# Performance work log

Hardware: AMD Instinct MI355X
Metric: run time of the kernel (lower is better)

The kernel has to match this reference:

```python
import jax, jax.numpy as jnp
import numpy as np

B, T, D, H = 2, 2048, 2048, 16
HD = D // H  # 128
HALF = HD // 2  # 64


def _apply_rotary(x, cos, sin):
    """x: (B,H,T,HD); cos/sin: (T, HD//2). Interleaved rotation matching torch ref."""
    half = x.shape[-1] // 2
    x1, x2 = x[..., :half], x[..., half:]
    c = cos[None, None, :, :]
    s = sin[None, None, :, :]
    # stack on last axis then flatten -> out[...,2i]=x1*c-x2*s, out[...,2i+1]=x1*s+x2*c
    return jnp.stack([x1 * c - x2 * s, x1 * s + x2 * c], axis=-1).reshape(x.shape)


def setup_inputs() -> dict:
    key = jax.random.key(0)
    k1, k2, k3 = jax.random.split(key, 3)
    x = jax.random.normal(k1, (B, T, D), dtype=jnp.float32)
    # realistic RoPE tables: theta = 10000^{-2i/HD}
    inv_freq = 1.0 / (10000.0 ** (np.arange(0, HALF, dtype=np.float32) * 2.0 / HD))
    ang = np.arange(T, dtype=np.float32)[:, None] * inv_freq[None, :]  # (T, HALF)
    cos = jnp.asarray(np.cos(ang), dtype=jnp.float32)
    sin = jnp.asarray(np.sin(ang), dtype=jnp.float32)
    Wqkv = jax.random.normal(k2, (D, 3 * D), dtype=jnp.float32) * (D ** -0.5)
    Wproj = jax.random.normal(k3, (D, D), dtype=jnp.float32) * (D ** -0.5)
    return {"x": x, "cos": cos, "sin": sin, "Wqkv": Wqkv, "Wproj": Wproj}


def reference(x, cos, sin, Wqkv, Wproj):
    b, t, d = x.shape
    qkv = (x @ Wqkv).reshape(b, t, 3, H, HD)
    q = jnp.transpose(qkv[:, :, 0], (0, 2, 1, 3))  # (B,H,T,HD)
    k = jnp.transpose(qkv[:, :, 1], (0, 2, 1, 3))
    v = jnp.transpose(qkv[:, :, 2], (0, 2, 1, 3))
    q = _apply_rotary(q, cos, sin)
    k = _apply_rotary(k, cos, sin)
    scale = 1.0 / jnp.sqrt(jnp.asarray(HD, dtype=x.dtype))
    scores = jnp.einsum("bhqd,bhkd->bhqk", q, k) * scale
    causal = jnp.tril(jnp.ones((t, t), dtype=bool))
    scores = jnp.where(causal[None, None], scores, jnp.finfo(x.dtype).min)
    attn = jax.nn.softmax(scores, axis=-1)
    out = jnp.einsum("bhqk,bhkd->bhqd", attn, v)
    out = jnp.transpose(out, (0, 2, 1, 3)).reshape(b, t, d)
    return out @ Wproj
```

## Files before the change

### kernel.cpp

```cpp
#include <hip/hip_runtime.h>
#include <hip/hip_bf16.h>

#define B_  2
#define T_  2048
#define D_  2048
#define H_  16
#define HD_ 128
#define NT_ 4096
#define D3_ 6144

typedef __bf16 bf16;
typedef _Float16 f16;
typedef bf16 bf16x2 __attribute__((ext_vector_type(2)));
typedef bf16 bf16x4 __attribute__((ext_vector_type(4)));
typedef bf16 bf16x8 __attribute__((ext_vector_type(8)));
typedef f16  f16x2  __attribute__((ext_vector_type(2)));
typedef f16  f16x4  __attribute__((ext_vector_type(4)));
typedef float floatx4 __attribute__((ext_vector_type(4)));

__device__ __forceinline__ void gl_lds16(const void* g, void* l) {
    __builtin_amdgcn_global_load_lds((const __attribute__((address_space(1))) void*)g,
                                     (__attribute__((address_space(3))) void*)l, 16, 0, 0);
}

__global__ __launch_bounds__(256) void k_prep(const float* __restrict__ x,
                                              const float* __restrict__ Wqkv, const float* __restrict__ Wproj,
                                              bf16* __restrict__ xb, bf16* __restrict__ WqkvT, bf16* __restrict__ WprojT) {
    int blk = blockIdx.x;
    int tid = threadIdx.x;
    if (blk < 8192) {
        int i = blk * 256 + tid;
        float4 v = ((const float4*)x)[i];
        bf16x4 o = { (bf16)v.x, (bf16)v.y, (bf16)v.z, (bf16)v.w };
        ((bf16x4*)xb)[i] = o;
        return;
    }
    __shared__ float tile[64][65];
    const float* in; bf16* out; int C, bx;
    if (blk < 8192 + 3072) { bx = blk - 8192; in = Wqkv; out = WqkvT; C = D3_; }
    else                   { bx = blk - 8192 - 3072; in = Wproj; out = WprojT; C = D_; }
    const int R = D_;
    int nbx = C / 64;
    int c0 = (bx % nbx) * 64, r0 = (bx / nbx) * 64;
#pragma unroll
    for (int i = 0; i < 16; i++) {
        int idx = tid + i * 256, r = idx >> 6, c = idx & 63;
        tile[r][c] = in[(size_t)(r0 + r) * C + (c0 + c)];
    }
    __syncthreads();
#pragma unroll
    for (int i = 0; i < 16; i++) {
        int idx = tid + i * 256, r = idx >> 6, c = idx & 63;
        out[(size_t)(c0 + r) * R + (r0 + c)] = (bf16)tile[c][r];
    }
}

__global__ __launch_bounds__(256) void k_gemm_qkv(const bf16* __restrict__ A, const bf16* __restrict__ Bt,
                                                  const float* __restrict__ cosp, const float* __restrict__ sinp,
                                                  bf16* __restrict__ Qg, bf16* __restrict__ Kg, f16* __restrict__ VTg) {
    __shared__ bf16 As[128 * 32];
    __shared__ bf16 Bs[128 * 32];
    __shared__ bf16 stage[128 * 130];
    const int tid = threadIdx.x, w = tid >> 6, lane = tid & 63;
    const int quad = lane >> 4, l16 = lane & 15;
    const int n0 = blockIdx.x * 128, m0 = blockIdx.y * 128;
    const int wr = (w >> 1) * 64, wc = (w & 1) * 64;
    const int srow = lane >> 2, schunk = (lane & 3) ^ ((lane >> 2) & 3);
    const bf16* Aw = A + (size_t)m0 * D_ + (size_t)(w * 32 + srow) * D_ + schunk * 8;
    const bf16* Bw = Bt + (size_t)n0 * D_ + (size_t)(w * 32 + srow) * D_ + schunk * 8;
    const int co = (quad ^ (l16 & 3)) * 8;
    const bf16* Abase = As + (wr + l16) * 32 + co;
    const bf16* Bbase = Bs + (wc + l16) * 32 + co;
    floatx4 acc[4][4] = {};
    for (int k0 = 0; k0 < D_; k0 += 32) {
        __syncthreads();
#pragma unroll
        for (int i = 0; i < 2; i++) {
            gl_lds16(Aw + k0 + i * 16 * D_, As + (w * 2 + i) * 512);
            gl_lds16(Bw + k0 + i * 16 * D_, Bs + (w * 2 + i) * 512);
        }
        __syncthreads();
        bf16x8 af[4], bfr[4];
#pragma unroll
        for (int mt = 0; mt < 4; mt++) af[mt] = *(const bf16x8*)(Abase + mt * 512);
#pragma unroll
        for (int nt = 0; nt < 4; nt++) bfr[nt] = *(const bf16x8*)(Bbase + nt * 512);
#pragma unroll
        for (int mt = 0; mt < 4; mt++)
#pragma unroll
            for (int nt = 0; nt < 4; nt++)
                acc[mt][nt] = __builtin_amdgcn_mfma_f32_16x16x32_bf16(af[mt], bfr[nt], acc[mt][nt], 0, 0, 0);
    }
    __syncthreads();
#pragma unroll
    for (int mt = 0; mt < 4; mt++)
#pragma unroll
        for (int nt = 0; nt < 4; nt++)
#pragma unroll
            for (int r = 0; r < 4; r++)
                stage[(wr + mt * 16 + quad * 4 + r) * 130 + wc + nt * 16 + l16] = (bf16)acc[mt][nt][r];
    __syncthreads();
    const int type = n0 >> 11, h = (n0 & 2047) >> 7;
    const int b = m0 >> 11, t0 = m0 & 2047;
    if (type < 2) {
        bf16* out = (type == 0 ? Qg : Kg) + ((size_t)(b * H_ + h) * T_ + t0) * HD_;
#pragma unroll
        for (int it = 0; it < 32; it++) {
            int idx = it * 256 + tid, tl = idx >> 6, i = idx & 63;
            float c = cosp[(t0 + tl) * 64 + i], s = sinp[(t0 + tl) * 64 + i];
            float x1 = (float)stage[tl * 130 + i], x2 = (float)stage[tl * 130 + 64 + i];
            bf16x2 o = { (bf16)(x1 * c - x2 * s), (bf16)(x1 * s + x2 * c) };
            *(bf16x2*)(out + (size_t)tl * HD_ + 2 * i) = o;
        }
    } else {
        f16* out = VTg + (size_t)(b * H_ + h) * HD_ * T_ + t0;
#pragma unroll
        for (int it = 0; it < 32; it++) {
            int idx = it * 256 + tid, d = idx >> 6, tp = (idx & 63) * 2;
            f16x2 o = { (f16)(float)stage[tp * 130 + d], (f16)(float)stage[(tp + 1) * 130 + d] };
            *(f16x2*)(out + (size_t)d * T_ + tp) = o;
        }
    }
}

template <typename OutT>
__global__ __launch_bounds__(256) void k_gemm_bt(const bf16* __restrict__ A, const bf16* __restrict__ Bt,
                                                 OutT* __restrict__ C, int M, int N, int K) {
    __shared__ bf16 As[128 * 64];
    __shared__ bf16 Bs[128 * 64];
    const int tid = threadIdx.x, w = tid >> 6, lane = tid & 63;
    const int quad = lane >> 4, l16 = lane & 15;
    const int x7 = l16 & 7;
    const int n0 = blockIdx.x * 128, m0 = blockIdx.y * 128;
    const int wr = (w >> 1) * 64, wc = (w & 1) * 64;
    const bf16* Ab = A + (size_t)m0 * K;
    const bf16* Bb = Bt + (size_t)n0 * K;
    const int srow = lane >> 3, schunk = (lane & 7) ^ (lane >> 3);
    floatx4 acc[4][4] = {};
    for (int k0 = 0; k0 < K; k0 += 64) {
        __syncthreads();
#pragma unroll
        for (int i = 0; i < 4; i++) {
            int ch = w * 4 + i;
            int row = ch * 8 + srow;
            gl_lds16(Ab + (size_t)row * K + k0 + schunk * 8, As + ch * 512);
            gl_lds16(Bb + (size_t)row * K + k0 + schunk * 8, Bs + ch * 512);
        }
        __syncthreads();
#pragma unroll
        for (int kc = 0; kc < 2; kc++) {
            const int co = ((kc * 4 + quad) ^ x7) * 8;
            const bf16* Abase = As + (wr + l16) * 64 + co;
            const bf16* Bbase = Bs + (wc + l16) * 64 + co;
            bf16x8 af[4], bfr[4];
#pragma unroll
            for (int mt = 0; mt < 4; mt++) af[mt] = *(const bf16x8*)(Abase + mt * 1024);
#pragma unroll
            for (int nt = 0; nt < 4; nt++) bfr[nt] = *(const bf16x8*)(Bbase + nt * 1024);
#pragma unroll
            for (int mt = 0; mt < 4; mt++)
#pragma unroll
                for (int nt = 0; nt < 4; nt++)
                    acc[mt][nt] = __builtin_amdgcn_mfma_f32_16x16x32_bf16(af[mt], bfr[nt], acc[mt][nt], 0, 0, 0);
        }
    }
#pragma unroll
    for (int mt = 0; mt < 4; mt++)
#pragma unroll
        for (int nt = 0; nt < 4; nt++)
#pragma unroll
            for (int r = 0; r < 4; r++) {
                int row = m0 + wr + mt * 16 + quad * 4 + r;
                int col = n0 + wc + nt * 16 + l16;
                C[(size_t)row * N + col] = (OutT)acc[mt][nt][r];
            }
}

__global__ __launch_bounds__(256, 2) void k_flash(const bf16* __restrict__ Qg, const bf16* __restrict__ Kg,
                                                  const f16* __restrict__ VTg, bf16* __restrict__ Og) {
    __shared__ bf16 Ksh[2][64 * 128];
    __shared__ f16  Vsh[2][128 * 64];
    const int b1 = blockIdx.x;
    const int bh = b1 & 31;
    const int qt = (b1 < 256) ? (15 - (b1 >> 5)) : ((b1 - 256) >> 5);
    const int tid = threadIdx.x, w = tid >> 6, lane = tid & 63;
    const int quad = lane >> 4, l16 = lane & 15;
    const float scale2 = 0.08838834764831845f * 1.4426950408889634f;
    const int wrow = w * 32;
    const bf16* Kb = Kg + (size_t)bh * T_ * HD_;
    const f16*  Vb = VTg + (size_t)bh * HD_ * T_;
    const int krow_ = (lane >> 4), kc_ = (lane & 15) ^ 0;
    const bf16* Qb = Qg + ((size_t)bh * T_ + qt * 128) * HD_;
    bf16x8 qf[2][4];
#pragma unroll
    for (int mt = 0; mt < 2; mt++)
#pragma unroll
        for (int kc = 0; kc < 4; kc++)
            qf[mt][kc] = *(const bf16x8*)(Qb + (size_t)(wrow + mt * 16 + l16) * HD_ + kc * 32 + quad * 8);
    floatx4 oaccT[8][2] = {};
    float lsum[2] = { 0.f, 0.f };
    const int nkt = 2 * (qt + 1);

    {
        const bf16* Kt = Kb;
        const f16*  Vt = Vb;
#pragma unroll
        for (int i = 0; i < 4; i++) {
            int ch = w * 4 + i;
            {
                int row = ch * 4 + (lane >> 4);
                int c = (lane & 15) ^ (row & 7);
                gl_lds16(Kt + (size_t)row * HD_ + c * 8, &Ksh[0][ch * 512]);
            }
            {
                int row = ch * 8 + (lane >> 3);
                int c = (lane & 7) ^ (row & 7);
                gl_lds16(Vt + (size_t)row * T_ + c * 8, &Vsh[0][ch * 512]);
            }
        }
    }
    int cur = 0;
    for (int kt = 0; kt < nkt; kt++) {
        __syncthreads();
        if (kt + 1 < nkt) {
            const bf16* Kt = Kb + (size_t)(kt + 1) * 64 * HD_;
            const f16*  Vt = Vb + (size_t)(kt + 1) * 64;
            const int nb = cur ^ 1;
#pragma unroll
            for (int i = 0; i < 4; i++) {
                int ch = w * 4 + i;
                {
                    int row = ch * 4 + (lane >> 4);
                    int c = (lane & 15) ^ (row & 7);
                    gl_lds16(Kt + (size_t)row * HD_ + c * 8, &Ksh[nb][ch * 512]);
                }
                {
                    int row = ch * 8 + (lane >> 3);
                    int c = (lane & 7) ^ (row & 7);
                    gl_lds16(Vt + (size_t)row * T_ + c * 8, &Vsh[nb][ch * 512]);
                }
            }
        }
        const bf16* Kcur = Ksh[cur];
        const f16*  Vcur = Vsh[cur];
        const bool diag = (kt >= 2 * qt);
        f16x4 pf[2][4];
#pragma unroll
        for (int nt = 0; nt < 4; nt++) {
            floatx4 s0 = {}, s1 = {};
#pragma unroll
            for (int kc = 0; kc < 4; kc++) {
                bf16x8 kf = *(const bf16x8*)(Kcur + (nt * 16 + l16) * 128 + (((kc * 4 + quad) ^ (l16 & 7)) * 8));
                s0 = __builtin_amdgcn_mfma_f32_16x16x32_bf16(kf, qf[0][kc], s0, 0, 0, 0);
                s1 = __builtin_amdgcn_mfma_f32_16x16x32_bf16(kf, qf[1][kc], s1, 0, 0, 0);
            }
#pragma unroll
            for (int r = 0; r < 4; r++) {
                float v0 = s0[r] * scale2, v1 = s1[r] * scale2;
                if (diag) {
                    int gk = kt * 64 + nt * 16 + quad * 4 + r;
                    if (gk > qt * 128 + wrow + l16) v0 = -1e30f;
                    if (gk > qt * 128 + wrow + 16 + l16) v1 = -1e30f;
                }
                float p0 = exp2f(v0), p1 = exp2f(v1);
                lsum[0] += p0; lsum[1] += p1;
                pf[0][nt][r] = (f16)p0; pf[1][nt][r] = (f16)p1;
            }
        }
#pragma unroll
        for (int nt = 0; nt < 4; nt++)
#pragma unroll
            for (int dt = 0; dt < 8; dt++) {
                int row = dt * 16 + l16;
                f16x4 vf = *(const f16x4*)(Vcur + row * 64 + (((nt * 2 + (quad >> 1)) ^ (row & 7)) * 8) + (quad & 1) * 4);
#pragma unroll
                for (int mt = 0; mt < 2; mt++)
                    oaccT[dt][mt] = __builtin_amdgcn_mfma_f32_16x16x16f16(vf, pf[mt][nt], oaccT[dt][mt], 0, 0, 0);
            }
        cur ^= 1;
    }
    const int b = bh >> 4, h = bh & 15;
    float inv[2];
#pragma unroll
    for (int mt = 0; mt < 2; mt++) {
        float l = lsum[mt];
        l += __shfl_xor(l, 16);
        l += __shfl_xor(l, 32);
        inv[mt] = 1.0f / l;
    }
#pragma unroll
    for (int mt = 0; mt < 2; mt++) {
        int t = qt * 128 + wrow + mt * 16 + l16;
#pragma unroll
        for (int dt = 0; dt < 8; dt++) {
            bf16x4 o;
#pragma unroll
            for (int r = 0; r < 4; r++) o[r] = (bf16)(oaccT[dt][mt][r] * inv[mt]);
            int c = h * HD_ + dt * 16 + quad * 4;
            *(bf16x4*)(Og + (size_t)(b * T_ + t) * D_ + c) = o;
        }
    }
}

extern "C" void kernel_launch(void* const* d_in, const int* in_sizes, int n_in,
                              void* d_out, int out_size, void* d_ws, size_t ws_size,
                              hipStream_t stream) {
    const float* x     = (const float*)d_in[0];
    const float* cosp  = (const float*)d_in[1];
    const float* sinp  = (const float*)d_in[2];
    const float* Wqkv  = (const float*)d_in[3];
    const float* Wproj = (const float*)d_in[4];
    float* out = (float*)d_out;
    char* ws = (char*)d_ws;
    bf16* xb     = (bf16*)(ws);
    bf16* WqkvT  = (bf16*)(ws + (size_t)(16u << 20));
    bf16* WprojT = (bf16*)(ws + (size_t)(40u << 20));
    bf16* Qg     = (bf16*)(ws + (size_t)(48u << 20));
    bf16* Kg     = (bf16*)(ws + (size_t)(64u << 20));
    f16*  VTg    = (f16*) (ws + (size_t)(80u << 20));
    bf16* Og     = xb;

    k_prep<<<dim3(8192 + 3072 + 1024), 256, 0, stream>>>(x, Wqkv, Wproj, xb, WqkvT, WprojT);
    k_gemm_qkv<<<dim3(D3_ / 128, NT_ / 128), 256, 0, stream>>>(xb, WqkvT, cosp, sinp, Qg, Kg, VTg);
    k_flash<<<dim3(512), 256, 0, stream>>>(Qg, Kg, VTg, Og);
    k_gemm_bt<float><<<dim3(D_ / 128, NT_ / 128), 256, 0, stream>>>(Og, WprojT, out, NT_, D_, D_);
}
```

Baseline: 379.2 us.

## Triple-buffer QKV GEMM with 256x128 tiles and prefetch-two pipeline

Rewrites the QKV projection GEMM to use 512-thread blocks computing 256x128 output tiles with a K-step of 64. LDS is split into three buffers, and global-to-LDS loads run two K-steps ahead, interleaved between the two halves of the MFMA work. Partial vmcnt waits, split barriers and s_setprio are used to overlap memory traffic with matrix math. The aim is to hide load latency and raise data reuse per block. In exchange it uses much more LDS and a single block per CU, and the waitcnt bookkeeping is fragile.

```diff
diff --git a/kernel.cpp b/kernel.cpp
--- a/kernel.cpp
+++ b/kernel.cpp
@@ -55,43 +55,93 @@
     }
 }
 
-__global__ __launch_bounds__(256) void k_gemm_qkv(const bf16* __restrict__ A, const bf16* __restrict__ Bt,
-                                                  const float* __restrict__ cosp, const float* __restrict__ sinp,
-                                                  bf16* __restrict__ Qg, bf16* __restrict__ Kg, f16* __restrict__ VTg) {
-    __shared__ bf16 As[128 * 32];
-    __shared__ bf16 Bs[128 * 32];
-    __shared__ bf16 stage[128 * 130];
-    const int tid = threadIdx.x, w = tid >> 6, lane = tid & 63;
+__global__ __launch_bounds__(512, 1) void k_gemm_qkv(const bf16* __restrict__ A, const bf16* __restrict__ Bt,
+                                                     const float* __restrict__ cosp, const float* __restrict__ sinp,
+                                                     bf16* __restrict__ Qg, bf16* __restrict__ Kg, f16* __restrict__ VTg) {
+    __shared__ bf16 smem[3 * 24576];
+    const int tid = threadIdx.x, wid = tid >> 6, lane = tid & 63;
     const int quad = lane >> 4, l16 = lane & 15;
-    const int n0 = blockIdx.x * 128, m0 = blockIdx.y * 128;
-    const int wr = (w >> 1) * 64, wc = (w & 1) * 64;
-    const int srow = lane >> 2, schunk = (lane & 3) ^ ((lane >> 2) & 3);
-    const bf16* Aw = A + (size_t)m0 * D_ + (size_t)(w * 32 + srow) * D_ + schunk * 8;
-    const bf16* Bw = Bt + (size_t)n0 * D_ + (size_t)(w * 32 + srow) * D_ + schunk * 8;
-    const int co = (quad ^ (l16 & 3)) * 8;
-    const bf16* Abase = As + (wr + l16) * 32 + co;
-    const bf16* Bbase = Bs + (wc + l16) * 32 + co;
+    const int n0 = blockIdx.x * 128, m0 = blockIdx.y * 256;
+    const int wr = (wid >> 1) * 64, wc = (wid & 1) * 64;
+    const bf16* Ablk = A + (size_t)m0 * D_;
+    const bf16* Bblk = Bt + (size_t)n0 * D_;
+    const int sgch = (lane & 7) ^ (lane >> 3);
+    const int aHalf = (wid >> 2) * 8192;
+    const int rAbase = ((wid >> 1) & 1) * 64;
+    const int coA = (rAbase + l16) * 64;
+    const int coB = 16384 + (wc + l16) * 64;
     floatx4 acc[4][4] = {};
-    for (int k0 = 0; k0 < D_; k0 += 32) {
-        __syncthreads();
-#pragma unroll
-        for (int i = 0; i < 2; i++) {
-            gl_lds16(Aw + k0 + i * 16 * D_, As + (w * 2 + i) * 512);
-            gl_lds16(Bw + k0 + i * 16 * D_, Bs + (w * 2 + i) * 512);
-        }
-        __syncthreads();
-        bf16x8 af[4], bfr[4];
-#pragma unroll
-        for (int mt = 0; mt < 4; mt++) af[mt] = *(const bf16x8*)(Abase + mt * 512);
-#pragma unroll
-        for (int nt = 0; nt < 4; nt++) bfr[nt] = *(const bf16x8*)(Bbase + nt * 512);
+
+#define QKV_STAGE(KT, BUFO, JJ) do {                                                    \
+        int cI_ = (JJ) * 512 + wid * 64 + lane;                                         \
+        const bf16* gsrc_;                                                              \
+        if ((JJ) < 4) gsrc_ = Ablk + (size_t)(cI_ >> 3) * D_ + (KT) * 64 + sgch * 8;    \
+        else          gsrc_ = Bblk + (size_t)((cI_ >> 3) - 256) * D_ + (KT) * 64 + sgch * 8; \
+        gl_lds16(gsrc_, smem + (BUFO) + ((JJ) * 512 + wid * 64) * 8);                   \
+    } while (0)
+
+#pragma unroll
+    for (int j = 0; j < 6; j++) QKV_STAGE(0, 0, j);
+#pragma unroll
+    for (int j = 0; j < 6; j++) QKV_STAGE(1, 24576, j);
+    asm volatile("s_waitcnt vmcnt(6)" ::: "memory");
+    __builtin_amdgcn_s_barrier();
+
+    int bcur = 0, bpre = 2;
+    for (int t = 0; t < 32; t++) {
+        const int bb = bcur * 24576;
+        const int po = bpre * 24576;
+        const int kpre = t + 2;
+        const bool dopre = (kpre < 32);
+        bf16x8 af[4][2], bfr0[2][2];
 #pragma unroll
         for (int mt = 0; mt < 4; mt++)
 #pragma unroll
-            for (int nt = 0; nt < 4; nt++)
-                acc[mt][nt] = __builtin_amdgcn_mfma_f32_16x16x32_bf16(af[mt], bfr[nt], acc[mt][nt], 0, 0, 0);
-    }
-    __syncthreads();
+            for (int kc = 0; kc < 2; kc++)
+                af[mt][kc] = *(const bf16x8*)(smem + bb + aHalf + coA + mt * 1024 + (((kc * 4 + quad) ^ (l16 & 7)) * 8));
+#pragma unroll
+        for (int nt = 0; nt < 2; nt++)
+#pragma unroll
+            for (int kc = 0; kc < 2; kc++)
+                bfr0[nt][kc] = *(const bf16x8*)(smem + bb + coB + nt * 1024 + (((kc * 4 + quad) ^ (l16 & 7)) * 8));
+        if (dopre) { QKV_STAGE(kpre, po, 0); QKV_STAGE(kpre, po, 1); QKV_STAGE(kpre, po, 4); }
+        __builtin_amdgcn_s_barrier();
+        __builtin_amdgcn_s_setprio(1);
+#pragma unroll
+        for (int mt = 0; mt < 4; mt++)
+#pragma unroll
+            for (int nt = 0; nt < 2; nt++)
+#pragma unroll
+                for (int kc = 0; kc < 2; kc++)
+                    acc[mt][nt] = __builtin_amdgcn_mfma_f32_16x16x32_bf16(af[mt][kc], bfr0[nt][kc], acc[mt][nt], 0, 0, 0);
+        __builtin_amdgcn_s_setprio(0);
+        __builtin_amdgcn_s_barrier();
+        bf16x8 bfr1[2][2];
+#pragma unroll
+        for (int nt = 0; nt < 2; nt++)
+#pragma unroll
+            for (int kc = 0; kc < 2; kc++)
+                bfr1[nt][kc] = *(const bf16x8*)(smem + bb + coB + (nt + 2) * 1024 + (((kc * 4 + quad) ^ (l16 & 7)) * 8));
+        if (dopre) { QKV_STAGE(kpre, po, 2); QKV_STAGE(kpre, po, 3); QKV_STAGE(kpre, po, 5); }
+        __builtin_amdgcn_s_barrier();
+        __builtin_amdgcn_s_setprio(1);
+#pragma unroll
+        for (int mt = 0; mt < 4; mt++)
+#pragma unroll
+            for (int nt = 0; nt < 2; nt++)
+#pragma unroll
+                for (int kc = 0; kc < 2; kc++)
+                    acc[mt][nt + 2] = __builtin_amdgcn_mfma_f32_16x16x32_bf16(af[mt][kc], bfr1[nt][kc], acc[mt][nt + 2], 0, 0, 0);
+        __builtin_amdgcn_s_setprio(0);
+        if (t == 30) asm volatile("s_waitcnt vmcnt(0)" ::: "memory");
+        else         asm volatile("s_waitcnt vmcnt(6)" ::: "memory");
+        __builtin_amdgcn_s_barrier();
+        bcur = (bcur == 2) ? 0 : bcur + 1;
+        bpre = (bpre == 2) ? 0 : bpre + 1;
+    }
+#undef QKV_STAGE
+
+    bf16* const stage = smem;
 #pragma unroll
     for (int mt = 0; mt < 4; mt++)
 #pragma unroll
@@ -106,7 +156,7 @@
         bf16* out = (type == 0 ? Qg : Kg) + ((size_t)(b * H_ + h) * T_ + t0) * HD_;
 #pragma unroll
         for (int it = 0; it < 32; it++) {
-            int idx = it * 256 + tid, tl = idx >> 6, i = idx & 63;
+            int idx = it * 512 + tid, tl = idx >> 6, i = idx & 63;
             float c = cosp[(t0 + tl) * 64 + i], s = sinp[(t0 + tl) * 64 + i];
             float x1 = (float)stage[tl * 130 + i], x2 = (float)stage[tl * 130 + 64 + i];
             bf16x2 o = { (bf16)(x1 * c - x2 * s), (bf16)(x1 * s + x2 * c) };
@@ -116,7 +166,7 @@
         f16* out = VTg + (size_t)(b * H_ + h) * HD_ * T_ + t0;
 #pragma unroll
         for (int it = 0; it < 32; it++) {
-            int idx = it * 256 + tid, d = idx >> 6, tp = (idx & 63) * 2;
+            int idx = it * 512 + tid, d = idx >> 7, tp = (idx & 127) * 2;
             f16x2 o = { (f16)(float)stage[tp * 130 + d], (f16)(float)stage[(tp + 1) * 130 + d] };
             *(f16x2*)(out + (size_t)d * T_ + tp) = o;
         }
@@ -189,7 +239,6 @@
     const int wrow = w * 32;
     const bf16* Kb = Kg + (size_t)bh * T_ * HD_;
     const f16*  Vb = VTg + (size_t)bh * HD_ * T_;
-    const int krow_ = (lane >> 4), kc_ = (lane & 15) ^ 0;
     const bf16* Qb = Qg + ((size_t)bh * T_ + qt * 128) * HD_;
     bf16x8 qf[2][4];
 #pragma unroll
@@ -321,7 +370,7 @@
     bf16* Og     = xb;
 
     k_prep<<<dim3(8192 + 3072 + 1024), 256, 0, stream>>>(x, Wqkv, Wproj, xb, WqkvT, WprojT);
-    k_gemm_qkv<<<dim3(D3_ / 128, NT_ / 128), 256, 0, stream>>>(xb, WqkvT, cosp, sinp, Qg, Kg, VTg);
+    k_gemm_qkv<<<dim3(D3_ / 128, NT_ / 256), 512, 0, stream>>>(xb, WqkvT, cosp, sinp, Qg, Kg, VTg);
     k_flash<<<dim3(512), 256, 0, stream>>>(Qg, Kg, VTg, Og);
     k_gemm_bt<float><<<dim3(D_ / 128, NT_ / 128), 256, 0, stream>>>(Og, WprojT, out, NT_, D_, D_);
 }
```

New measurement: 377.6 us. Within noise of the previous version (-0.4%).
